# Performance work log

Hardware: AMD Instinct MI355X
Metric: run time of the kernel (lower is better)

The kernel has to match this reference:

```python
import jax, jax.numpy as jnp
import numpy as np

SEQ_LEN = 180
LATENT = 128
HIDDEN = 256
BATCH = 8192


def setup_inputs() -> dict:
    key = jax.random.key(0)
    ks = jax.random.split(key, 9)
    s = 1.0 / np.sqrt(HIDDEN)
    return {
        "z": jax.random.normal(ks[0], (BATCH, LATENT), jnp.float32),
        "fc_w": jax.random.normal(ks[1], (HIDDEN, LATENT), jnp.float32) * (1.0 / np.sqrt(LATENT)),
        "fc_b": jax.random.normal(ks[2], (HIDDEN,), jnp.float32) * 0.1,
        "w_ih": jax.random.normal(ks[3], (3 * HIDDEN, 2), jnp.float32) * s,
        "b_ih": jax.random.normal(ks[4], (3 * HIDDEN,), jnp.float32) * s,
        "w_hh": jax.random.normal(ks[5], (3 * HIDDEN, HIDDEN), jnp.float32) * s,
        "b_hh": jax.random.normal(ks[6], (3 * HIDDEN,), jnp.float32) * s,
        "out_w": jax.random.normal(ks[7], (2, HIDDEN), jnp.float32) * s,
        "out_b": jax.random.normal(ks[8], (2,), jnp.float32) * 0.1,
    }


def reference(z, fc_w, fc_b, w_ih, b_ih, w_hh, b_hh, out_w, out_b):
    # h0 = tanh(fc(z))  -> [B, H]
    h0 = jnp.tanh(z @ fc_w.T + fc_b)
    B = z.shape[0]
    # GRU input is all-zeros, so input-hidden gates are a constant bias: [B, 3H]
    gi = jnp.zeros((B, 2), z.dtype) @ w_ih.T + b_ih
    gi_r, gi_z, gi_n = jnp.split(gi, 3, axis=-1)

    def step(h, _):
        gh = h @ w_hh.T + b_hh                 # [B, 3H]
        gh_r, gh_z, gh_n = jnp.split(gh, 3, axis=-1)
        r = jax.nn.sigmoid(gi_r + gh_r)
        zg = jax.nn.sigmoid(gi_z + gh_z)
        n = jnp.tanh(gi_n + r * gh_n)
        h_new = (1.0 - zg) * n + zg * h
        return h_new, h_new

    _, hs = jax.lax.scan(step, h0, None, length=SEQ_LEN)  # [T, B, H]
    hs = jnp.swapaxes(hs, 0, 1)                            # [B, T, H]
    return hs @ out_w.T + out_b                            # [B, T, 2]
```

## Files before the change

### kernel.cpp

```cpp
#include <hip/hip_runtime.h>
#include <hip/hip_bf16.h>

#define T_SEQ  180
#define LATENT 128
#define HIDDEN 256

typedef __attribute__((ext_vector_type(8))) short  short8;
typedef __attribute__((ext_vector_type(4))) float  floatx4;
typedef __attribute__((ext_vector_type(4))) int    intx4;
typedef __attribute__((ext_vector_type(2))) float  float2v;

#define LOG2E 1.4426950408889634f

#define WQ_OFF    0
#define FCW_OFF   196608
#define SCW_OFF   262144
#define OUTW_OFF  265216
#define SWOUT_OFF 269312

#define H8_STRIDE  272
#define H8B_OFF    8704
#define OBUF_OFF   17408
#define SMEM_BYTES 18432

__device__ __forceinline__ unsigned short f2bf(float f) {
    unsigned int u = __float_as_uint(f);
    u += 0x7fffu + ((u >> 16) & 1u);
    return (unsigned short)(u >> 16);
}

__global__ void pack_scales(const float* __restrict__ whh, float* __restrict__ scales) {
    int wid  = blockIdx.x * 4 + (threadIdx.x >> 6);
    int lane = threadIdx.x & 63;
    const float* src = whh + (size_t)wid * 256 + lane * 4;
    float m = 0.0f;
#pragma unroll
    for (int j = 0; j < 4; ++j) m = fmaxf(m, fabsf(src[j]));
#pragma unroll
    for (int d = 1; d < 64; d <<= 1) m = fmaxf(m, __shfl_xor(m, d, 64));
    if (lane == 0) scales[wid] = m;
}

__global__ void pack_whh_i8(const float* __restrict__ whh, const float* __restrict__ scales,
                            signed char* __restrict__ dst) {
    int tid  = blockIdx.x * blockDim.x + threadIdx.x;
    int lane = tid & 63;
    int frag = tid >> 6;
    int kc   = frag & 3;
    int sub  = (frag >> 2) % 6;
    int w    = frag / 24;
    int g = sub >> 1, cs = sub & 1;
    int col  = w * 32 + cs * 16 + (lane & 15);
    int jout = g * 256 + col;
    int k0   = kc * 64 + ((lane >> 4) << 4);
    const float* src = whh + (size_t)jout * 256 + k0;
    float inv = 127.0f / scales[jout];
    signed char q[16];
#pragma unroll
    for (int j = 0; j < 16; ++j) {
        float v = __builtin_rintf(src[j] * inv);
        v = fminf(fmaxf(v, -127.0f), 127.0f);
        q[j] = (signed char)(int)v;
    }
    *(intx4*)(dst + (size_t)frag * 1024 + lane * 16) = *(intx4*)q;
}

__global__ void pack_fcw(const float* __restrict__ fcw, unsigned short* __restrict__ dst) {
    int tid  = blockIdx.x * blockDim.x + threadIdx.x;
    int lane = tid & 63;
    int frag = tid >> 6;
    int kc   = frag & 3;
    int cs   = (frag >> 2) & 1;
    int w    = frag >> 3;
    int col  = w * 32 + cs * 16 + (lane & 15);
    int k0   = kc * 32 + ((lane >> 4) << 3);
    const float* src = fcw + col * 128 + k0;
    unsigned int u[4];
#pragma unroll
    for (int j = 0; j < 4; ++j)
        u[j] = (unsigned int)f2bf(src[2 * j]) | ((unsigned int)f2bf(src[2 * j + 1]) << 16);
    *(uint4*)(dst + frag * 512 + lane * 8) = make_uint4(u[0], u[1], u[2], u[3]);
}

__global__ void pack_outw_i8(const float* __restrict__ out_w,
                             signed char* __restrict__ dst, float* __restrict__ swout) {
    __shared__ float sw[2];
    int tid = threadIdx.x;
    if (tid < 128) {
        int o = tid >> 6, lane = tid & 63;
        const float* src = out_w + o * 256 + lane * 4;
        float m = 0.0f;
#pragma unroll
        for (int j = 0; j < 4; ++j) m = fmaxf(m, fabsf(src[j]));
#pragma unroll
        for (int d = 1; d < 64; d <<= 1) m = fmaxf(m, __shfl_xor(m, d, 64));
        if (lane == 0) { sw[o] = m; swout[o] = m; }
    }
    __syncthreads();
    int sl = tid >> 6, lane = tid & 63;
    int n  = lane & 15;
    int k0 = sl * 64 + ((lane >> 4) << 4);
    signed char q[16];
#pragma unroll
    for (int j = 0; j < 16; ++j) {
        float v = 0.0f;
        if (n < 2) {
            v = __builtin_rintf(out_w[n * 256 + k0 + j] * (127.0f / sw[n]));
            v = fminf(fmaxf(v, -127.0f), 127.0f);
        }
        q[j] = (signed char)(int)v;
    }
    *(intx4*)(dst + sl * 1024 + lane * 16) = *(intx4*)q;
}

__global__ __launch_bounds__(1024, 4) void gru_main(
    const float* __restrict__ z,
    const float* __restrict__ fc_b,
    const float* __restrict__ b_ih,
    const float* __restrict__ b_hh,
    const float* __restrict__ out_b,
    const unsigned char* __restrict__ ws,
    float* __restrict__ out)
{
    extern __shared__ unsigned char smem[];
    signed char* h8a   = (signed char*)smem;
    signed char* h8b   = (signed char*)(smem + H8B_OFF);
    int*         obufI = (int*)(smem + OBUF_OFF);

    const int tid  = threadIdx.x;
    const int lane = tid & 63;
    const int wv   = tid >> 6;
    const int cg   = wv;
    const int l15  = lane & 15;
    const int qd   = lane >> 4;
    const int rh   = (wv >> 2) & 1;
    const int sl   = wv & 3;
    const int rb   = blockIdx.x * 32;
    const int wsw  = (l15 >> 2) & 3;

    const intx4 zero4 = (intx4){0, 0, 0, 0};

    intx4 wq[12];
#pragma unroll
    for (int g = 0; g < 3; ++g)
#pragma unroll
        for (int kc = 0; kc < 4; ++kc)
            wq[g * 4 + kc] = *(const intx4*)(ws + WQ_OFF
                + (size_t)((((cg >> 1) * 6 + g * 2 + (cg & 1)) * 4 + kc)) * 1024 + lane * 16);

    intx4 bproj = *(const intx4*)(ws + OUTW_OFF + sl * 1024 + lane * 16);
    const float* swout = (const float*)(ws + SWOUT_OFF);
    float pscF = swout[lane & 1] * (1.0f / 16129.0f);

    const float* scales = (const float*)(ws + SCW_OFF);
    float fcbE2;
    float2v nscqr2, ncbr2, nscqz2, ncbz2, scqn2, bhn2, bin2;
    {
        int col = cg * 16 + l15;
        float ncbrE  = -(b_ih[col]       + b_hh[col])       * LOG2E;
        float ncbzE  = -(b_ih[256 + col] + b_hh[256 + col]) * LOG2E;
        float binE2  = b_ih[512 + col] * (2.0f * LOG2E);
        float bhnE2  = b_hh[512 + col] * (2.0f * LOG2E);
        fcbE2  = fc_b[col] * (2.0f * LOG2E);
        float nscqrE = -scales[col]       * (LOG2E / 16129.0f);
        float nscqzE = -scales[256 + col] * (LOG2E / 16129.0f);
        float scqnE2 = scales[512 + col] * (2.0f * LOG2E / 16129.0f);
        nscqr2 = (float2v){nscqrE, nscqrE};  ncbr2 = (float2v){ncbrE, ncbrE};
        nscqz2 = (float2v){nscqzE, nscqzE};  ncbz2 = (float2v){ncbzE, ncbzE};
        scqn2  = (float2v){scqnE2, scqnE2};  bhn2  = (float2v){bhnE2, bhnE2};
        bin2   = (float2v){binE2, binE2};
    }
    const float2v m254 = (float2v){-254.0f, -254.0f};
    const float2v p127 = (float2v){127.0f, 127.0f};
    float ob = out_b[lane & 1];

    const int rdOff = l15 * H8_STRIDE + (qd ^ wsw) * 16;
    const int pjOff = (rh * 16 + l15) * H8_STRIDE + sl * 64 + (qd ^ wsw) * 16;
    const int wrOff = (qd * 4) * H8_STRIDE + ((cg ^ qd) & 15) * 16 + l15;

    const int rlW = ((wv - 8) * 4 + (lane >> 1)) & 31;
    const int o8  = lane & 1;
    const int fbase = (rlW >> 4) * 128 + (rlW & 15) * 2 + o8;
    float* opW8 = out + (size_t)(rb + rlW) * (T_SEQ * 2) + o8;

    floatx4 a0f[2];
#pragma unroll
    for (int rt = 0; rt < 2; ++rt) a0f[rt] = (floatx4){0.f, 0.f, 0.f, 0.f};
#pragma unroll
    for (int kc = 0; kc < 4; ++kc) {
        short8 bfr = *(const short8*)(ws + FCW_OFF + (size_t)(cg * 4 + kc) * 1024 + lane * 16);
#pragma unroll
        for (int rt = 0; rt < 2; ++rt) {
            const float* zp = z + (size_t)(rb + rt * 16 + l15) * LATENT + kc * 32 + qd * 8;
            short8 afr;
#pragma unroll
            for (int j = 0; j < 8; ++j) afr[j] = (short)f2bf(zp[j]);
            a0f[rt] = __builtin_amdgcn_mfma_f32_16x16x32_bf16(afr, bfr, a0f[rt], 0, 0, 0);
        }
    }

    float2v hm2[2][2];
#pragma unroll
    for (int rt = 0; rt < 2; ++rt)
#pragma unroll
        for (int r = 0; r < 4; ++r) {
            float u = __builtin_amdgcn_rcpf(1.0f + __builtin_amdgcn_exp2f(
                          __builtin_fmaf(a0f[rt][r], 2.0f * LOG2E, fcbE2)));
            float h = __builtin_fmaf(-254.0f, u, 127.0f);
            hm2[rt][r >> 1][r & 1] = h;
            h8a[wrOff + rt * (16 * H8_STRIDE) + r * H8_STRIDE] =
                (signed char)__float_as_uint(h + 12582912.0f);
        }
    __syncthreads();

    intx4 acc0[3], acc1[3];

#define HUPD_PAIR(ACC, RT, P, WP)                                                 \
    {                                                                             \
        float2v arv, azv, anv;                                                    \
        arv[0] = (float)(ACC)[0][2*(P)];   arv[1] = (float)(ACC)[0][2*(P)+1];     \
        azv[0] = (float)(ACC)[1][2*(P)];   azv[1] = (float)(ACC)[1][2*(P)+1];     \
        anv[0] = (float)(ACC)[2][2*(P)];   anv[1] = (float)(ACC)[2][2*(P)+1];     \
        float2v yr = __builtin_elementwise_fma(arv, nscqr2, ncbr2);               \
        float2v yz = __builtin_elementwise_fma(azv, nscqz2, ncbz2);               \
        float2v Ar, Az;                                                           \
        Ar[0] = __builtin_amdgcn_exp2f(yr[0]); Ar[1] = __builtin_amdgcn_exp2f(yr[1]); \
        Az[0] = __builtin_amdgcn_exp2f(yz[0]); Az[1] = __builtin_amdgcn_exp2f(yz[1]); \
        float2v dr = Ar + 1.0f, dz = Az + 1.0f;                                   \
        float2v pr = dr * dz;                                                     \
        float2v q_;                                                               \
        q_[0] = __builtin_amdgcn_rcpf(pr[0]); q_[1] = __builtin_amdgcn_rcpf(pr[1]); \
        float2v gr = q_ * dz, gz = q_ * dr;                                       \
        float2v xn2 = __builtin_elementwise_fma(anv, scqn2, bhn2);                \
        float2v tt  = __builtin_elementwise_fma(gr, xn2, bin2);                   \
        float2v Ee, uu;                                                           \
        Ee[0] = __builtin_amdgcn_exp2f(tt[0]); Ee[1] = __builtin_amdgcn_exp2f(tt[1]); \
        Ee = Ee + 1.0f;                                                           \
        uu[0] = __builtin_amdgcn_rcpf(Ee[0]); uu[1] = __builtin_amdgcn_rcpf(Ee[1]); \
        float2v gn = __builtin_elementwise_fma(m254, uu, p127);                   \
        float2v hv = hm2[RT][P];                                                  \
        float2v hn = __builtin_elementwise_fma(gz, hv - gn, gn);                  \
        hm2[RT][P] = hn;                                                          \
        float2v hb = hn + 12582912.0f;                                            \
        (WP)[(2*(P))   * H8_STRIDE] = (signed char)__float_as_uint(hb[0]);        \
        (WP)[(2*(P)+1) * H8_STRIDE] = (signed char)__float_as_uint(hb[1]);        \
    }

#define REGION_A(BUF, DO_V1, DO_FLUSH)                                           \
    {                                                                            \
        const signed char* rp = (BUF) + rdOff;                                   \
        signed char*       wp = (BUF) + wrOff + 16 * H8_STRIDE;                  \
        intx4 a8 = *(const intx4*)(rp);                                          \
        acc0[0] = __builtin_amdgcn_mfma_i32_16x16x64_i8(a8, wq[0], zero4,   0, 0, 0); \
        acc0[1] = __builtin_amdgcn_mfma_i32_16x16x64_i8(a8, wq[4], zero4,   0, 0, 0); \
        acc0[2] = __builtin_amdgcn_mfma_i32_16x16x64_i8(a8, wq[8], zero4,   0, 0, 0); \
        if (DO_V1) { HUPD_PAIR(acc1, 1, 0, wp) }                                 \
        a8 = *(const intx4*)(rp + 64);                                           \
        acc0[0] = __builtin_amdgcn_mfma_i32_16x16x64_i8(a8, wq[1], acc0[0], 0, 0, 0); \
        acc0[1] = __builtin_amdgcn_mfma_i32_16x16x64_i8(a8, wq[5], acc0[1], 0, 0, 0); \
        acc0[2] = __builtin_amdgcn_mfma_i32_16x16x64_i8(a8, wq[9], acc0[2], 0, 0, 0); \
        if (DO_V1) { HUPD_PAIR(acc1, 1, 1, wp) }                                 \
        a8 = *(const intx4*)(rp + 128);                                          \
        acc0[0] = __builtin_amdgcn_mfma_i32_16x16x64_i8(a8, wq[2], acc0[0], 0, 0, 0); \
        acc0[1] = __builtin_amdgcn_mfma_i32_16x16x64_i8(a8, wq[6], acc0[1], 0, 0, 0); \
        acc0[2] = __builtin_amdgcn_mfma_i32_16x16x64_i8(a8, wq[10], acc0[2], 0, 0, 0); \
        if (DO_FLUSH && wv >= 8 && lane < 8) {                                   \
            int s_ = obufI[fbase] + obufI[fbase + 32]                            \
                   + obufI[fbase + 64] + obufI[fbase + 96];                      \
            *opW8 = __builtin_fmaf((float)s_, pscF, ob);                         \
            opW8 += 2;                                                           \
        }                                                                        \
        a8 = *(const intx4*)(rp + 192);                                          \
        acc0[0] = __builtin_amdgcn_mfma_i32_16x16x64_i8(a8, wq[3], acc0[0], 0, 0, 0); \
        acc0[1] = __builtin_amdgcn_mfma_i32_16x16x64_i8(a8, wq[7], acc0[1], 0, 0, 0); \
        acc0[2] = __builtin_amdgcn_mfma_i32_16x16x64_i8(a8, wq[11], acc0[2], 0, 0, 0); \
        __syncthreads();                                                         \
    }

#define REGION_C(BUFR, BUFW, DO_PJ)                                              \
    {                                                                            \
        const signed char* rp = (BUFR) + rdOff + 16 * H8_STRIDE;                 \
        signed char*       wp = (BUFW) + wrOff;                                  \
        intx4 pj;                                                                \
        if (DO_PJ && wv < 8) {                                                   \
            intx4 a8p = *(const intx4*)((BUFR) + pjOff);                         \
            pj = __builtin_amdgcn_mfma_i32_16x16x64_i8(a8p, bproj, zero4, 0, 0, 0); \
        }                                                                        \
        intx4 a8 = *(const intx4*)(rp);                                          \
        acc1[0] = __builtin_amdgcn_mfma_i32_16x16x64_i8(a8, wq[0], zero4,   0, 0, 0); \
        acc1[1] = __builtin_amdgcn_mfma_i32_16x16x64_i8(a8, wq[4], zero4,   0, 0, 0); \
        acc1[2] = __builtin_amdgcn_mfma_i32_16x16x64_i8(a8, wq[8], zero4,   0, 0, 0); \
        HUPD_PAIR(acc0, 0, 0, wp)                                                \
        a8 = *(const intx4*)(rp + 64);                                           \
        acc1[0] = __builtin_amdgcn_mfma_i32_16x16x64_i8(a8, wq[1], acc1[0], 0, 0, 0); \
        acc1[1] = __builtin_amdgcn_mfma_i32_16x16x64_i8(a8, wq[5], acc1[1], 0, 0, 0); \
        acc1[2] = __builtin_amdgcn_mfma_i32_16x16x64_i8(a8, wq[9], acc1[2], 0, 0, 0); \
        HUPD_PAIR(acc0, 0, 1, wp)                                                \
        a8 = *(const intx4*)(rp + 128);                                          \
        acc1[0] = __builtin_amdgcn_mfma_i32_16x16x64_i8(a8, wq[2], acc1[0], 0, 0, 0); \
        acc1[1] = __builtin_amdgcn_mfma_i32_16x16x64_i8(a8, wq[6], acc1[1], 0, 0, 0); \
        acc1[2] = __builtin_amdgcn_mfma_i32_16x16x64_i8(a8, wq[10], acc1[2], 0, 0, 0); \
        a8 = *(const intx4*)(rp + 192);                                          \
        acc1[0] = __builtin_amdgcn_mfma_i32_16x16x64_i8(a8, wq[3], acc1[0], 0, 0, 0); \
        acc1[1] = __builtin_amdgcn_mfma_i32_16x16x64_i8(a8, wq[7], acc1[1], 0, 0, 0); \
        acc1[2] = __builtin_amdgcn_mfma_i32_16x16x64_i8(a8, wq[11], acc1[2], 0, 0, 0); \
        if (DO_PJ && wv < 8 && l15 < 2) {                                        \
            _Pragma("unroll")                                                    \
            for (int r = 0; r < 4; ++r)                                          \
                obufI[(rh * 4 + sl) * 32 + (qd * 4 + r) * 2 + l15] = pj[r];      \
        }                                                                        \
        __syncthreads();                                                         \
    }

    REGION_A(h8a, 0, 0)
    REGION_C(h8a, h8b, 0)
    REGION_A(h8b, 1, 0)
    REGION_C(h8b, h8a, 1)

#pragma unroll 1
    for (int t2 = 0; t2 < 89; ++t2) {
        REGION_A(h8a, 1, 1)
        REGION_C(h8a, h8b, 1)
        REGION_A(h8b, 1, 1)
        REGION_C(h8b, h8a, 1)
    }

    {
        signed char* wp = h8a + wrOff + 16 * H8_STRIDE;
        HUPD_PAIR(acc1, 1, 0, wp)
        HUPD_PAIR(acc1, 1, 1, wp)
        if (wv >= 8 && lane < 8) {
            int s_ = obufI[fbase] + obufI[fbase + 32]
                   + obufI[fbase + 64] + obufI[fbase + 96];
            *opW8 = __builtin_fmaf((float)s_, pscF, ob);
            opW8 += 2;
        }
        __syncthreads();
    }
    if (wv < 8) {
        intx4 a8p = *(const intx4*)(h8a + pjOff);
        intx4 pj = __builtin_amdgcn_mfma_i32_16x16x64_i8(a8p, bproj, zero4, 0, 0, 0);
        if (l15 < 2)
#pragma unroll
            for (int r = 0; r < 4; ++r)
                obufI[(rh * 4 + sl) * 32 + (qd * 4 + r) * 2 + l15] = pj[r];
    }
    __syncthreads();
    if (wv >= 8 && lane < 8) {
        int s_ = obufI[fbase] + obufI[fbase + 32]
               + obufI[fbase + 64] + obufI[fbase + 96];
        *opW8 = __builtin_fmaf((float)s_, pscF, ob);
    }
#undef REGION_C
#undef REGION_A
#undef HUPD_PAIR
}

extern "C" void kernel_launch(void* const* d_in, const int* in_sizes, int n_in,
                              void* d_out, int out_size, void* d_ws, size_t ws_size,
                              hipStream_t stream) {
    const float* z     = (const float*)d_in[0];
    const float* fc_w  = (const float*)d_in[1];
    const float* fc_b  = (const float*)d_in[2];
    const float* b_ih  = (const float*)d_in[4];
    const float* w_hh  = (const float*)d_in[5];
    const float* b_hh  = (const float*)d_in[6];
    const float* out_w = (const float*)d_in[7];
    const float* out_b = (const float*)d_in[8];
    float* out = (float*)d_out;
    unsigned char* ws = (unsigned char*)d_ws;

    hipFuncSetAttribute((const void*)gru_main,
                        hipFuncAttributeMaxDynamicSharedMemorySize, SMEM_BYTES);

    pack_scales<<<192, 256, 0, stream>>>(w_hh, (float*)(ws + SCW_OFF));
    pack_whh_i8<<<48, 256, 0, stream>>>(w_hh, (const float*)(ws + SCW_OFF),
                                        (signed char*)(ws + WQ_OFF));
    pack_fcw<<<16, 256, 0, stream>>>(fc_w, (unsigned short*)(ws + FCW_OFF));
    pack_outw_i8<<<1, 256, 0, stream>>>(out_w, (signed char*)(ws + OUTW_OFF),
                                        (float*)(ws + SWOUT_OFF));
    gru_main<<<256, 1024, SMEM_BYTES, stream>>>(z, fc_b, b_ih, b_hh, out_b, ws, out);
}
```

Measured before the change: 463.2 us.

## Merge half-step regions into one barrier per GRU step with double-buffered output stash

```diff
diff --git a/kernel.cpp b/kernel.cpp
--- a/kernel.cpp
+++ b/kernel.cpp
@@ -21,7 +21,8 @@
 #define H8_STRIDE  272
 #define H8B_OFF    8704
 #define OBUF_OFF   17408
-#define SMEM_BYTES 18432
+#define OBUF_HALF  256
+#define SMEM_BYTES 19456
 
 __device__ __forceinline__ unsigned short f2bf(float f) {
     unsigned int u = __float_as_uint(f);
@@ -246,113 +247,98 @@
         (WP)[(2*(P)+1) * H8_STRIDE] = (signed char)__float_as_uint(hb[1]);        \
     }
 
-#define REGION_A(BUF, DO_V1, DO_FLUSH)                                           \
+#define GRU_STEP(H8P, H8N, OBR, OBW, DO_STASH, DO_FLUSH)                         \
     {                                                                            \
-        const signed char* rp = (BUF) + rdOff;                                   \
-        signed char*       wp = (BUF) + wrOff + 16 * H8_STRIDE;                  \
-        intx4 a8 = *(const intx4*)(rp);                                          \
+        const signed char* rp0 = (H8P) + rdOff;                                  \
+        const signed char* rp1 = rp0 + 16 * H8_STRIDE;                           \
+        signed char*       wp0 = (H8N) + wrOff;                                  \
+        signed char*       wp1 = wp0 + 16 * H8_STRIDE;                           \
+        intx4 pj;                                                                \
+        if (DO_STASH && wv < 8) {                                                \
+            intx4 a8p = *(const intx4*)((H8P) + pjOff);                          \
+            pj = __builtin_amdgcn_mfma_i32_16x16x64_i8(a8p, bproj, zero4, 0, 0, 0); \
+        }                                                                        \
+        if (DO_FLUSH && wv >= 8 && lane < 8) {                                   \
+            int s_ = (OBR)[fbase] + (OBR)[fbase + 32]                            \
+                   + (OBR)[fbase + 64] + (OBR)[fbase + 96];                      \
+            *opW8 = __builtin_fmaf((float)s_, pscF, ob);                         \
+            opW8 += 2;                                                           \
+        }                                                                        \
+        intx4 a8 = *(const intx4*)(rp0);                                         \
         acc0[0] = __builtin_amdgcn_mfma_i32_16x16x64_i8(a8, wq[0], zero4,   0, 0, 0); \
         acc0[1] = __builtin_amdgcn_mfma_i32_16x16x64_i8(a8, wq[4], zero4,   0, 0, 0); \
         acc0[2] = __builtin_amdgcn_mfma_i32_16x16x64_i8(a8, wq[8], zero4,   0, 0, 0); \
-        if (DO_V1) { HUPD_PAIR(acc1, 1, 0, wp) }                                 \
-        a8 = *(const intx4*)(rp + 64);                                           \
+        a8 = *(const intx4*)(rp1);                                               \
+        acc1[0] = __builtin_amdgcn_mfma_i32_16x16x64_i8(a8, wq[0], zero4,   0, 0, 0); \
+        acc1[1] = __builtin_amdgcn_mfma_i32_16x16x64_i8(a8, wq[4], zero4,   0, 0, 0); \
+        acc1[2] = __builtin_amdgcn_mfma_i32_16x16x64_i8(a8, wq[8], zero4,   0, 0, 0); \
+        a8 = *(const intx4*)(rp0 + 64);                                          \
         acc0[0] = __builtin_amdgcn_mfma_i32_16x16x64_i8(a8, wq[1], acc0[0], 0, 0, 0); \
         acc0[1] = __builtin_amdgcn_mfma_i32_16x16x64_i8(a8, wq[5], acc0[1], 0, 0, 0); \
         acc0[2] = __builtin_amdgcn_mfma_i32_16x16x64_i8(a8, wq[9], acc0[2], 0, 0, 0); \
-        if (DO_V1) { HUPD_PAIR(acc1, 1, 1, wp) }                                 \
-        a8 = *(const intx4*)(rp + 128);                                          \
+        a8 = *(const intx4*)(rp1 + 64);                                          \
+        acc1[0] = __builtin_amdgcn_mfma_i32_16x16x64_i8(a8, wq[1], acc1[0], 0, 0, 0); \
+        acc1[1] = __builtin_amdgcn_mfma_i32_16x16x64_i8(a8, wq[5], acc1[1], 0, 0, 0); \
+        acc1[2] = __builtin_amdgcn_mfma_i32_16x16x64_i8(a8, wq[9], acc1[2], 0, 0, 0); \
+        a8 = *(const intx4*)(rp0 + 128);                                         \
         acc0[0] = __builtin_amdgcn_mfma_i32_16x16x64_i8(a8, wq[2], acc0[0], 0, 0, 0); \
         acc0[1] = __builtin_amdgcn_mfma_i32_16x16x64_i8(a8, wq[6], acc0[1], 0, 0, 0); \
         acc0[2] = __builtin_amdgcn_mfma_i32_16x16x64_i8(a8, wq[10], acc0[2], 0, 0, 0); \
-        if (DO_FLUSH && wv >= 8 && lane < 8) {                                   \
-            int s_ = obufI[fbase] + obufI[fbase + 32]                            \
-                   + obufI[fbase + 64] + obufI[fbase + 96];                      \
-            *opW8 = __builtin_fmaf((float)s_, pscF, ob);                         \
-            opW8 += 2;                                                           \
-        }                                                                        \
-        a8 = *(const intx4*)(rp + 192);                                          \
+        a8 = *(const intx4*)(rp1 + 128);                                         \
+        acc1[0] = __builtin_amdgcn_mfma_i32_16x16x64_i8(a8, wq[2], acc1[0], 0, 0, 0); \
+        acc1[1] = __builtin_amdgcn_mfma_i32_16x16x64_i8(a8, wq[6], acc1[1], 0, 0, 0); \
+        acc1[2] = __builtin_amdgcn_mfma_i32_16x16x64_i8(a8, wq[10], acc1[2], 0, 0, 0); \
+        a8 = *(const intx4*)(rp0 + 192);                                         \
         acc0[0] = __builtin_amdgcn_mfma_i32_16x16x64_i8(a8, wq[3], acc0[0], 0, 0, 0); \
         acc0[1] = __builtin_amdgcn_mfma_i32_16x16x64_i8(a8, wq[7], acc0[1], 0, 0, 0); \
         acc0[2] = __builtin_amdgcn_mfma_i32_16x16x64_i8(a8, wq[11], acc0[2], 0, 0, 0); \
-        __syncthreads();                                                         \
-    }
-
-#define REGION_C(BUFR, BUFW, DO_PJ)                                              \
-    {                                                                            \
-        const signed char* rp = (BUFR) + rdOff + 16 * H8_STRIDE;                 \
-        signed char*       wp = (BUFW) + wrOff;                                  \
-        intx4 pj;                                                                \
-        if (DO_PJ && wv < 8) {                                                   \
-            intx4 a8p = *(const intx4*)((BUFR) + pjOff);                         \
-            pj = __builtin_amdgcn_mfma_i32_16x16x64_i8(a8p, bproj, zero4, 0, 0, 0); \
-        }                                                                        \
-        intx4 a8 = *(const intx4*)(rp);                                          \
-        acc1[0] = __builtin_amdgcn_mfma_i32_16x16x64_i8(a8, wq[0], zero4,   0, 0, 0); \
-        acc1[1] = __builtin_amdgcn_mfma_i32_16x16x64_i8(a8, wq[4], zero4,   0, 0, 0); \
-        acc1[2] = __builtin_amdgcn_mfma_i32_16x16x64_i8(a8, wq[8], zero4,   0, 0, 0); \
-        HUPD_PAIR(acc0, 0, 0, wp)                                                \
-        a8 = *(const intx4*)(rp + 64);                                           \
-        acc1[0] = __builtin_amdgcn_mfma_i32_16x16x64_i8(a8, wq[1], acc1[0], 0, 0, 0); \
-        acc1[1] = __builtin_amdgcn_mfma_i32_16x16x64_i8(a8, wq[5], acc1[1], 0, 0, 0); \
-        acc1[2] = __builtin_amdgcn_mfma_i32_16x16x64_i8(a8, wq[9], acc1[2], 0, 0, 0); \
-        HUPD_PAIR(acc0, 0, 1, wp)                                                \
-        a8 = *(const intx4*)(rp + 128);                                          \
-        acc1[0] = __builtin_amdgcn_mfma_i32_16x16x64_i8(a8, wq[2], acc1[0], 0, 0, 0); \
-        acc1[1] = __builtin_amdgcn_mfma_i32_16x16x64_i8(a8, wq[6], acc1[1], 0, 0, 0); \
-        acc1[2] = __builtin_amdgcn_mfma_i32_16x16x64_i8(a8, wq[10], acc1[2], 0, 0, 0); \
-        a8 = *(const intx4*)(rp + 192);                                          \
+        a8 = *(const intx4*)(rp1 + 192);                                         \
         acc1[0] = __builtin_amdgcn_mfma_i32_16x16x64_i8(a8, wq[3], acc1[0], 0, 0, 0); \
         acc1[1] = __builtin_amdgcn_mfma_i32_16x16x64_i8(a8, wq[7], acc1[1], 0, 0, 0); \
         acc1[2] = __builtin_amdgcn_mfma_i32_16x16x64_i8(a8, wq[11], acc1[2], 0, 0, 0); \
-        if (DO_PJ && wv < 8 && l15 < 2) {                                        \
+        HUPD_PAIR(acc0, 0, 0, wp0)                                               \
+        HUPD_PAIR(acc0, 0, 1, wp0)                                               \
+        HUPD_PAIR(acc1, 1, 0, wp1)                                               \
+        HUPD_PAIR(acc1, 1, 1, wp1)                                               \
+        if (DO_STASH && wv < 8 && l15 < 2) {                                     \
             _Pragma("unroll")                                                    \
             for (int r = 0; r < 4; ++r)                                          \
-                obufI[(rh * 4 + sl) * 32 + (qd * 4 + r) * 2 + l15] = pj[r];      \
+                (OBW)[(rh * 4 + sl) * 32 + (qd * 4 + r) * 2 + l15] = pj[r];      \
         }                                                                        \
         __syncthreads();                                                         \
     }
 
-    REGION_A(h8a, 0, 0)
-    REGION_C(h8a, h8b, 0)
-    REGION_A(h8b, 1, 0)
-    REGION_C(h8b, h8a, 1)
+    int* ob0 = obufI;
+    int* ob1 = obufI + OBUF_HALF;
+
+    GRU_STEP(h8a, h8b, ob1, ob0, 0, 0)
+    GRU_STEP(h8b, h8a, ob0, ob1, 1, 0)
 
 #pragma unroll 1
     for (int t2 = 0; t2 < 89; ++t2) {
-        REGION_A(h8a, 1, 1)
-        REGION_C(h8a, h8b, 1)
-        REGION_A(h8b, 1, 1)
-        REGION_C(h8b, h8a, 1)
-    }
-
-    {
-        signed char* wp = h8a + wrOff + 16 * H8_STRIDE;
-        HUPD_PAIR(acc1, 1, 0, wp)
-        HUPD_PAIR(acc1, 1, 1, wp)
-        if (wv >= 8 && lane < 8) {
-            int s_ = obufI[fbase] + obufI[fbase + 32]
-                   + obufI[fbase + 64] + obufI[fbase + 96];
-            *opW8 = __builtin_fmaf((float)s_, pscF, ob);
-            opW8 += 2;
-        }
-        __syncthreads();
-    }
+        GRU_STEP(h8a, h8b, ob1, ob0, 1, 1)
+        GRU_STEP(h8b, h8a, ob0, ob1, 1, 1)
+    }
+
     if (wv < 8) {
         intx4 a8p = *(const intx4*)(h8a + pjOff);
         intx4 pj = __builtin_amdgcn_mfma_i32_16x16x64_i8(a8p, bproj, zero4, 0, 0, 0);
         if (l15 < 2)
 #pragma unroll
             for (int r = 0; r < 4; ++r)
-                obufI[(rh * 4 + sl) * 32 + (qd * 4 + r) * 2 + l15] = pj[r];
+                ob0[(rh * 4 + sl) * 32 + (qd * 4 + r) * 2 + l15] = pj[r];
+    }
+    if (wv >= 8 && lane < 8) {
+        int s_ = ob1[fbase] + ob1[fbase + 32] + ob1[fbase + 64] + ob1[fbase + 96];
+        *opW8 = __builtin_fmaf((float)s_, pscF, ob);
+        opW8 += 2;
     }
     __syncthreads();
     if (wv >= 8 && lane < 8) {
-        int s_ = obufI[fbase] + obufI[fbase + 32]
-               + obufI[fbase + 64] + obufI[fbase + 96];
+        int s_ = ob0[fbase] + ob0[fbase + 32] + ob0[fbase + 64] + ob0[fbase + 96];
         *opW8 = __builtin_fmaf((float)s_, pscF, ob);
     }
-#undef REGION_C
-#undef REGION_A
+#undef GRU_STEP
 #undef HUPD_PAIR
 }
 
```

After: 474.4 us. 1.02x slower.
